# Kernel optimization log

Measured on AMD Instinct MI355X. Metric: run time of the kernel, lower is better.

The kernel has to match this reference:

```python
import jax, jax.numpy as jnp
import numpy as np

B, T, D_IN, D_OUT = 8, 2048, 4096, 4096
N_ADAPTERS, R_MAX = 8, 64


def setup_inputs() -> dict:
    key = jax.random.key(0)
    k_x, k_base, k_idx, k_A, k_B, k_s = jax.random.split(key, 6)
    x = jax.random.normal(k_x, (B, T, D_IN), dtype=jnp.float32)
    base_output = jax.random.normal(k_base, (B, T, D_OUT), dtype=jnp.float32)
    adapter_indices = jax.random.randint(k_idx, (B,), 0, N_ADAPTERS, dtype=jnp.int64)
    # He-uniform init for A (kaiming_uniform with a=sqrt(5) -> bound = 1/sqrt(fan_in))
    bound = 1.0 / np.sqrt(D_IN)
    lora_A = jax.random.uniform(k_A, (N_ADAPTERS, D_IN, R_MAX), dtype=jnp.float32,
                                minval=-bound, maxval=bound)
    # lora_B is zeros at init; use small random values for a non-trivial reference
    lora_B = jax.random.normal(k_B, (N_ADAPTERS, R_MAX, D_OUT), dtype=jnp.float32) * 0.02
    lora_scaling = jax.random.uniform(k_s, (N_ADAPTERS,), dtype=jnp.float32,
                                      minval=0.5, maxval=2.0)
    return {"x": x, "base_output": base_output, "adapter_indices": adapter_indices,
            "lora_A": lora_A, "lora_B": lora_B, "lora_scaling": lora_scaling}


def reference(x, base_output, adapter_indices, lora_A, lora_B, lora_scaling):
    # Gather per-batch adapter weights (adapter index broadcasts over sequence):
    # equivalent to sort-by-adapter -> grouped GEMM -> unsort, since every token
    # in a batch row shares one adapter and all ranks equal r_max.
    A_b = lora_A[adapter_indices]          # [B, D_IN, R]
    B_b = lora_B[adapter_indices]          # [B, R, D_OUT]
    s_b = lora_scaling[adapter_indices]    # [B]
    inter = jnp.einsum('btd,bdr->btr', x, A_b)        # [B, T, R]
    y = jnp.einsum('btr,bro->bto', inter, B_b)        # [B, T, D_OUT]
    return base_output + y * s_b[:, None, None]
```

## Files before the change

kernel.cpp:

```cpp
#include <hip/hip_runtime.h>
#include <hip/hip_bf16.h>
#include <cstdint>
#include <cstddef>

#define BT    16384
#define DIN   4096
#define DOUT  4096
#define RR    64
#define TSEQ  2048
#define NADP  8

typedef float  f32x4  __attribute__((ext_vector_type(4)));
typedef __bf16 bf16x8 __attribute__((ext_vector_type(8)));

static __device__ __forceinline__ unsigned short bf16_bits(float f) {
    return __builtin_bit_cast(unsigned short, (__bf16)f);
}

static __device__ __forceinline__ size_t i2_idx(int mblk, int rb, int mrow, int j) {
    return ((((size_t)mblk * 8 + rb) * 16 + mrow) * 8 + j);
}

static __device__ __forceinline__ bf16x8 cvt8(float4 a, float4 b) {
    bf16x8 v;
    v[0] = (__bf16)a.x; v[1] = (__bf16)a.y; v[2] = (__bf16)a.z; v[3] = (__bf16)a.w;
    v[4] = (__bf16)b.x; v[5] = (__bf16)b.y; v[6] = (__bf16)b.z; v[7] = (__bf16)b.w;
    return v;
}

static __device__ __forceinline__ bf16x8 cvt8v(f32x4 a, f32x4 b) {
    bf16x8 v;
    v[0] = (__bf16)a[0]; v[1] = (__bf16)a[1]; v[2] = (__bf16)a[2]; v[3] = (__bf16)a[3];
    v[4] = (__bf16)b[0]; v[5] = (__bf16)b[1]; v[6] = (__bf16)b[2]; v[7] = (__bf16)b[3];
    return v;
}

typedef const __attribute__((address_space(1))) void* gas1_t;
typedef __attribute__((address_space(3))) void*       gas3_t;
static __device__ __forceinline__ void gll16(const void* g, void* l) {
    __builtin_amdgcn_global_load_lds((gas1_t)(uintptr_t)g,
                                     (gas3_t)(uint32_t)(uintptr_t)l,
                                     16, 0, 0);
}

__global__ __launch_bounds__(256) void k_prep_a(
    const float* __restrict__ A, __bf16* __restrict__ At2)
{
    const int gtid = blockIdx.x * 256 + threadIdx.x;
    const int r  = gtid & 63;
    const int kb = (gtid >> 6) & (DIN / 8 - 1);
    const int a  = gtid >> 15;
    const float* __restrict__ src = A + (size_t)a * DIN * RR + (size_t)kb * 8 * RR + r;
    unsigned int u[4];
    #pragma unroll
    for (int p = 0; p < 4; ++p) {
        unsigned int lo = bf16_bits(src[(2 * p + 0) * RR]);
        unsigned int hi = bf16_bits(src[(2 * p + 1) * RR]);
        u[p] = lo | (hi << 16);
    }
    *(uint4*)&At2[(size_t)gtid * 8] = make_uint4(u[0], u[1], u[2], u[3]);
}

__global__ __launch_bounds__(256) void k_prep_b(
    const float* __restrict__ Bw, __bf16* __restrict__ Bp)
{
    const int gtid = blockIdx.x * 256 + threadIdx.x;
    const int o  = gtid & (DOUT - 1);
    const int rb = (gtid >> 12) & 7;
    const int a  = gtid >> 15;
    const float* __restrict__ src = Bw + (size_t)a * RR * DOUT + (size_t)rb * 8 * DOUT + o;
    unsigned int u[4];
    #pragma unroll
    for (int p = 0; p < 4; ++p) {
        unsigned int lo = bf16_bits(src[(2 * p + 0) * DOUT]);
        unsigned int hi = bf16_bits(src[(2 * p + 1) * DOUT]);
        u[p] = lo | (hi << 16);
    }
    *(uint4*)&Bp[(size_t)gtid * 8] = make_uint4(u[0], u[1], u[2], u[3]);
}

__global__ __launch_bounds__(256, 2) void k_xa(
    const float* __restrict__ x, const int* __restrict__ idx,
    const __bf16* __restrict__ At2, __bf16* __restrict__ inter2)
{
    __shared__ float xs[2][32][64];

    const int m0   = blockIdx.x * 32;
    const int a    = idx[m0 / TSEQ];
    const int w    = threadIdx.x >> 6, lane = threadIdx.x & 63;
    const int mr   = lane & 15, kg = lane >> 4;
    const int rcol = w * 16 + mr;

    const __bf16* __restrict__ Aw = At2 + (size_t)a * RR * DIN;

    const float* gsrc0;
    const float* gsrc1;
    {
        const int R0 = w * 8 + 0 * 4 + kg;
        const int R1 = w * 8 + 1 * 4 + kg;
        const int s0 = (lane & 15) ^ (R0 & 15);
        const int s1 = (lane & 15) ^ (R1 & 15);
        gsrc0 = x + (size_t)(m0 + R0) * DIN + s0 * 4;
        gsrc1 = x + (size_t)(m0 + R1) * DIN + s1 * 4;
    }

    f32x4 z = {0.f, 0.f, 0.f, 0.f};
    f32x4 acc0 = z, acc1 = z;

#define STAGE(B, T)                                                      \
    {                                                                    \
        gll16(gsrc0 + (T) * 64, &xs[B][w * 8 + 0][0]);                   \
        gll16(gsrc1 + (T) * 64, &xs[B][w * 8 + 4][0]);                   \
    }

#define COMPUTE(B, T)                                                              \
    {                                                                              \
        _Pragma("unroll")                                                          \
        for (int ksub = 0; ksub < 2; ++ksub) {                                     \
            const int kq = ksub * 4 + kg;                                          \
            bf16x8 bfw = *(const bf16x8*)&Aw[(((size_t)(T) * 8 + kq) * 64 + rcol) * 8]; \
            f32x4 lo0 = *(const f32x4*)&xs[B][mr]     [((2 * kq)     ^ mr) * 4];   \
            f32x4 hi0 = *(const f32x4*)&xs[B][mr]     [((2 * kq + 1) ^ mr) * 4];   \
            f32x4 lo1 = *(const f32x4*)&xs[B][16 + mr][((2 * kq)     ^ mr) * 4];   \
            f32x4 hi1 = *(const f32x4*)&xs[B][16 + mr][((2 * kq + 1) ^ mr) * 4];   \
            acc0 = __builtin_amdgcn_mfma_f32_16x16x32_bf16(cvt8v(lo0, hi0), bfw, acc0, 0, 0, 0); \
            acc1 = __builtin_amdgcn_mfma_f32_16x16x32_bf16(cvt8v(lo1, hi1), bfw, acc1, 0, 0, 0); \
        }                                                                          \
    }

    STAGE(0, 0)
    __syncthreads();

    for (int t = 0; t < 63; ++t) {
        STAGE((t + 1) & 1, t + 1)
        COMPUTE(t & 1, t)
        __syncthreads();
    }
    COMPUTE(1, 63)

#undef STAGE
#undef COMPUTE

    const int rb = w * 2 + (mr >> 3), j = mr & 7;
    #pragma unroll
    for (int q = 0; q < 4; ++q) {
        inter2[i2_idx(blockIdx.x * 2 + 0, rb, kg * 4 + q, j)] = (__bf16)acc0[q];
        inter2[i2_idx(blockIdx.x * 2 + 1, rb, kg * 4 + q, j)] = (__bf16)acc1[q];
    }
}

__global__ __launch_bounds__(256) void k_by(
    const __bf16* __restrict__ inter2, const float* __restrict__ base,
    const int* __restrict__ idx, const __bf16* __restrict__ Bp,
    const float* __restrict__ scal, float* __restrict__ out)
{
    const int o0 = blockIdx.x * 64;
    const int m0 = blockIdx.y * 64;
    const int a  = idx[m0 / TSEQ];
    const float s = scal[a];
    const __bf16* __restrict__ Ba = Bp + (size_t)a * RR * DOUT;
    const int lane = threadIdx.x & 63;
    const int w    = threadIdx.x >> 6;
    const int mr   = lane & 15, kg = lane >> 4;
    const int oc   = o0 + w * 16 + mr;

    f32x4 z = {0.f, 0.f, 0.f, 0.f};
    f32x4 acc[4] = {z, z, z, z};

    #pragma unroll
    for (int ksub = 0; ksub < 2; ++ksub) {
        const int rb = ksub * 4 + kg;
        bf16x8 bfA = *(const bf16x8*)&Ba[((size_t)rb * DOUT + oc) * 8];
        #pragma unroll
        for (int mt = 0; mt < 4; ++mt) {
            bf16x8 afB = *(const bf16x8*)&inter2[i2_idx(m0 / 16 + mt, rb, mr, 0)];
            acc[mt] = __builtin_amdgcn_mfma_f32_16x16x32_bf16(bfA, afB, acc[mt], 0, 0, 0);
        }
    }

    #pragma unroll
    for (int mt = 0; mt < 4; ++mt) {
        size_t off = (size_t)(m0 + mt * 16 + mr) * DOUT + o0 + w * 16 + kg * 4;
        float4 bv = *(const float4*)&base[off];
        float4 o;
        o.x = bv.x + s * acc[mt][0];
        o.y = bv.y + s * acc[mt][1];
        o.z = bv.z + s * acc[mt][2];
        o.w = bv.w + s * acc[mt][3];
        *(float4*)&out[off] = o;
    }
}

__global__ __launch_bounds__(256) void k_xa_fb(
    const float* __restrict__ x, const int* __restrict__ idx,
    const float* __restrict__ A, __bf16* __restrict__ inter)
{
    const int m0   = blockIdx.x * 32;
    const int a    = idx[m0 / TSEQ];
    const float* __restrict__ Aa = A + (size_t)a * DIN * RR;
    const int lane = threadIdx.x & 63;
    const int rw   = threadIdx.x >> 6;
    const int mr   = lane & 15, kg = lane >> 4;
    const int rcol = rw * 16 + mr;
    const float* __restrict__ xrow0 = x + (size_t)(m0 + mr) * DIN;
    const float* __restrict__ xrow1 = x + (size_t)(m0 + 16 + mr) * DIN;

    f32x4 acc0 = {0.f, 0.f, 0.f, 0.f};
    f32x4 acc1 = {0.f, 0.f, 0.f, 0.f};

    for (int k0 = 0; k0 < DIN; k0 += 64) {
        #pragma unroll
        for (int ksub = 0; ksub < 2; ++ksub) {
            const int koff = k0 + ksub * 32 + kg * 8;
            float4 u0 = *(const float4*)&xrow0[koff];
            float4 u1 = *(const float4*)&xrow0[koff + 4];
            float4 v0 = *(const float4*)&xrow1[koff];
            float4 v1 = *(const float4*)&xrow1[koff + 4];
            bf16x8 af0 = cvt8(u0, u1);
            bf16x8 af1 = cvt8(v0, v1);
            const float* ap = &Aa[(size_t)koff * RR + rcol];
            bf16x8 bf;
            bf[0] = (__bf16)ap[0 * RR]; bf[1] = (__bf16)ap[1 * RR];
            bf[2] = (__bf16)ap[2 * RR]; bf[3] = (__bf16)ap[3 * RR];
            bf[4] = (__bf16)ap[4 * RR]; bf[5] = (__bf16)ap[5 * RR];
            bf[6] = (__bf16)ap[6 * RR]; bf[7] = (__bf16)ap[7 * RR];
            acc0 = __builtin_amdgcn_mfma_f32_16x16x32_bf16(af0, bf, acc0, 0, 0, 0);
            acc1 = __builtin_amdgcn_mfma_f32_16x16x32_bf16(af1, bf, acc1, 0, 0, 0);
        }
    }
    #pragma unroll
    for (int q = 0; q < 4; ++q) {
        inter[(size_t)(m0 + kg * 4 + q) * RR + rcol]      = (__bf16)acc0[q];
        inter[(size_t)(m0 + 16 + kg * 4 + q) * RR + rcol] = (__bf16)acc1[q];
    }
}

__global__ __launch_bounds__(256) void k_by_fb(
    const __bf16* __restrict__ inter, const float* __restrict__ base,
    const int* __restrict__ idx, const float* __restrict__ Bw,
    const float* __restrict__ scal, float* __restrict__ out)
{
    const int o0 = blockIdx.x * 64;
    const int m0 = blockIdx.y * 64;
    const int a  = idx[m0 / TSEQ];
    const float s = scal[a];
    const float* __restrict__ Ba = Bw + (size_t)a * RR * DOUT;
    const int lane = threadIdx.x & 63;
    const int w    = threadIdx.x >> 6;
    const int mr   = lane & 15, kg = lane >> 4;
    const int oc   = o0 + w * 16 + mr;

    f32x4 z = {0.f, 0.f, 0.f, 0.f};
    f32x4 acc[4] = {z, z, z, z};

    #pragma unroll
    for (int ksub = 0; ksub < 2; ++ksub) {
        const int kb = ksub * 32 + kg * 8;
        const float* bp = &Ba[(size_t)kb * DOUT + oc];
        bf16x8 bf;
        bf[0] = (__bf16)bp[0 * DOUT]; bf[1] = (__bf16)bp[1 * DOUT];
        bf[2] = (__bf16)bp[2 * DOUT]; bf[3] = (__bf16)bp[3 * DOUT];
        bf[4] = (__bf16)bp[4 * DOUT]; bf[5] = (__bf16)bp[5 * DOUT];
        bf[6] = (__bf16)bp[6 * DOUT]; bf[7] = (__bf16)bp[7 * DOUT];
        #pragma unroll
        for (int mt = 0; mt < 4; ++mt) {
            bf16x8 af = *(const bf16x8*)&inter[(size_t)(m0 + mt * 16 + mr) * RR + kb];
            acc[mt] = __builtin_amdgcn_mfma_f32_16x16x32_bf16(af, bf, acc[mt], 0, 0, 0);
        }
    }
    #pragma unroll
    for (int mt = 0; mt < 4; ++mt) {
        #pragma unroll
        for (int q = 0; q < 4; ++q) {
            size_t off = (size_t)(m0 + mt * 16 + kg * 4 + q) * DOUT + oc;
            out[off] = base[off] + s * acc[mt][q];
        }
    }
}

extern "C" void kernel_launch(void* const* d_in, const int* in_sizes, int n_in,
                              void* d_out, int out_size, void* d_ws, size_t ws_size,
                              hipStream_t stream)
{
    const float* x    = (const float*)d_in[0];
    const float* base = (const float*)d_in[1];
    const int*   idx  = (const int*)  d_in[2];
    const float* A    = (const float*)d_in[3];
    const float* Bw   = (const float*)d_in[4];
    const float* scal = (const float*)d_in[5];
    float* out = (float*)d_out;

    const size_t INTER_B = (size_t)BT * RR * 2;
    const size_t AT_B    = (size_t)NADP * RR * DIN * 2;
    const size_t BT_B    = (size_t)NADP * DOUT * RR * 2;

    if (ws_size >= INTER_B + AT_B + BT_B) {
        __bf16* inter2 = (__bf16*)d_ws;
        __bf16* At2    = (__bf16*)((char*)d_ws + INTER_B);
        __bf16* Bp     = (__bf16*)((char*)d_ws + INTER_B + AT_B);
        k_prep_a<<<dim3(1024), 256, 0, stream>>>(A, At2);
        k_prep_b<<<dim3(1024), 256, 0, stream>>>(Bw, Bp);
        k_xa<<<dim3(BT / 32),            256, 0, stream>>>(x, idx, At2, inter2);
        k_by<<<dim3(DOUT / 64, BT / 64), 256, 0, stream>>>(inter2, base, idx, Bp, scal, out);
    } else {
        __bf16* inter = (__bf16*)d_ws;
        k_xa_fb<<<dim3(BT / 32),            256, 0, stream>>>(x, idx, A, inter);
        k_by_fb<<<dim3(DOUT / 64, BT / 64), 256, 0, stream>>>(inter, base, idx, Bw, scal, out);
    }
}
```

Before: 206.8 us.

## Shrink x@A tile to 16 rows with register-staged loads and higher occupancy

Halves the row tile of the x·A kernel from 32 to 16 rows, doubling the grid and raising the launch-bounds occupancy hint from 2 to 4 blocks per CU. It replaces the async global_load_lds staging with plain vector loads into registers followed by stores to shared memory, one 16-byte chunk per thread. The aim is more parallelism to hide latency on this memory-bound stage. In exchange, each A-weight fragment is reused across only one MFMA tile instead of two, which doubles A reads, and the register-staged loads are no longer asynchronous.

Result: no change. 207.2 us (+0.2%).

```diff
diff --git a/kernel.cpp b/kernel.cpp
--- a/kernel.cpp
+++ b/kernel.cpp
@@ -35,14 +35,6 @@
     return v;
 }
 
-typedef const __attribute__((address_space(1))) void* gas1_t;
-typedef __attribute__((address_space(3))) void*       gas3_t;
-static __device__ __forceinline__ void gll16(const void* g, void* l) {
-    __builtin_amdgcn_global_load_lds((gas1_t)(uintptr_t)g,
-                                     (gas3_t)(uint32_t)(uintptr_t)l,
-                                     16, 0, 0);
-}
-
 __global__ __launch_bounds__(256) void k_prep_a(
     const float* __restrict__ A, __bf16* __restrict__ At2)
 {
@@ -79,13 +71,13 @@
     *(uint4*)&Bp[(size_t)gtid * 8] = make_uint4(u[0], u[1], u[2], u[3]);
 }
 
-__global__ __launch_bounds__(256, 2) void k_xa(
+__global__ __launch_bounds__(256, 4) void k_xa(
     const float* __restrict__ x, const int* __restrict__ idx,
     const __bf16* __restrict__ At2, __bf16* __restrict__ inter2)
 {
-    __shared__ float xs[2][32][64];
-
-    const int m0   = blockIdx.x * 32;
+    __shared__ float xs[2][16][64];
+
+    const int m0   = blockIdx.x * 16;
     const int a    = idx[m0 / TSEQ];
     const int w    = threadIdx.x >> 6, lane = threadIdx.x & 63;
     const int mr   = lane & 15, kg = lane >> 4;
@@ -93,39 +85,30 @@
 
     const __bf16* __restrict__ Aw = At2 + (size_t)a * RR * DIN;
 
-    const float* gsrc0;
-    const float* gsrc1;
-    {
-        const int R0 = w * 8 + 0 * 4 + kg;
-        const int R1 = w * 8 + 1 * 4 + kg;
-        const int s0 = (lane & 15) ^ (R0 & 15);
-        const int s1 = (lane & 15) ^ (R1 & 15);
-        gsrc0 = x + (size_t)(m0 + R0) * DIN + s0 * 4;
-        gsrc1 = x + (size_t)(m0 + R1) * DIN + s1 * 4;
-    }
-
-    f32x4 z = {0.f, 0.f, 0.f, 0.f};
-    f32x4 acc0 = z, acc1 = z;
-
-#define STAGE(B, T)                                                      \
-    {                                                                    \
-        gll16(gsrc0 + (T) * 64, &xs[B][w * 8 + 0][0]);                   \
-        gll16(gsrc1 + (T) * 64, &xs[B][w * 8 + 4][0]);                   \
-    }
-
-#define COMPUTE(B, T)                                                              \
-    {                                                                              \
-        _Pragma("unroll")                                                          \
-        for (int ksub = 0; ksub < 2; ++ksub) {                                     \
-            const int kq = ksub * 4 + kg;                                          \
+    const int sr = threadIdx.x >> 4;
+    const int so = threadIdx.x & 15;
+    const float* __restrict__ gsrc = x + (size_t)(m0 + sr) * DIN + (so ^ sr) * 4;
+    float* const d0 = &xs[0][sr][so * 4];
+    float* const d1 = &xs[1][sr][so * 4];
+
+    f32x4 acc = {0.f, 0.f, 0.f, 0.f};
+
+#define STAGE(B, T)                                                     \
+    {                                                                   \
+        f32x4 sv = *(const f32x4*)(gsrc + (T) * 64);                    \
+        *(f32x4*)((B) ? d1 : d0) = sv;                                  \
+    }
+
+#define COMPUTE(B, T)                                                             \
+    {                                                                             \
+        _Pragma("unroll")                                                         \
+        for (int kstep = 0; kstep < 2; ++kstep) {                                 \
+            const int kq = kstep * 4 + kg;                                        \
             bf16x8 bfw = *(const bf16x8*)&Aw[(((size_t)(T) * 8 + kq) * 64 + rcol) * 8]; \
-            f32x4 lo0 = *(const f32x4*)&xs[B][mr]     [((2 * kq)     ^ mr) * 4];   \
-            f32x4 hi0 = *(const f32x4*)&xs[B][mr]     [((2 * kq + 1) ^ mr) * 4];   \
-            f32x4 lo1 = *(const f32x4*)&xs[B][16 + mr][((2 * kq)     ^ mr) * 4];   \
-            f32x4 hi1 = *(const f32x4*)&xs[B][16 + mr][((2 * kq + 1) ^ mr) * 4];   \
-            acc0 = __builtin_amdgcn_mfma_f32_16x16x32_bf16(cvt8v(lo0, hi0), bfw, acc0, 0, 0, 0); \
-            acc1 = __builtin_amdgcn_mfma_f32_16x16x32_bf16(cvt8v(lo1, hi1), bfw, acc1, 0, 0, 0); \
-        }                                                                          \
+            f32x4 lo = *(const f32x4*)&xs[B][mr][((2 * kq)     ^ mr) * 4];        \
+            f32x4 hi = *(const f32x4*)&xs[B][mr][((2 * kq + 1) ^ mr) * 4];        \
+            acc = __builtin_amdgcn_mfma_f32_16x16x32_bf16(cvt8v(lo, hi), bfw, acc, 0, 0, 0); \
+        }                                                                         \
     }
 
     STAGE(0, 0)
@@ -143,10 +126,8 @@
 
     const int rb = w * 2 + (mr >> 3), j = mr & 7;
     #pragma unroll
-    for (int q = 0; q < 4; ++q) {
-        inter2[i2_idx(blockIdx.x * 2 + 0, rb, kg * 4 + q, j)] = (__bf16)acc0[q];
-        inter2[i2_idx(blockIdx.x * 2 + 1, rb, kg * 4 + q, j)] = (__bf16)acc1[q];
-    }
+    for (int q = 0; q < 4; ++q)
+        inter2[i2_idx(blockIdx.x, rb, kg * 4 + q, j)] = (__bf16)acc[q];
 }
 
 __global__ __launch_bounds__(256) void k_by(
@@ -300,7 +281,7 @@
         __bf16* Bp     = (__bf16*)((char*)d_ws + INTER_B + AT_B);
         k_prep_a<<<dim3(1024), 256, 0, stream>>>(A, At2);
         k_prep_b<<<dim3(1024), 256, 0, stream>>>(Bw, Bp);
-        k_xa<<<dim3(BT / 32),            256, 0, stream>>>(x, idx, At2, inter2);
+        k_xa<<<dim3(BT / 16),            256, 0, stream>>>(x, idx, At2, inter2);
         k_by<<<dim3(DOUT / 64, BT / 64), 256, 0, stream>>>(inter2, base, idx, Bp, scal, out);
     } else {
         __bf16* inter = (__bf16*)d_ws;
```
